# Optimization experiments

Measured on AMD Instinct MI355X. Metric: run time of the kernel, lower is better.

## Reference

```python
import jax, jax.numpy as jnp
import numpy as np

T, H, NH, NKV, HD = 2048, 1024, 16, 4, 64
I, E, TOPK = 2048, 8, 2
EPS = 1e-5
ROPE_BASE = 10000.0


def rms_norm(x, w):
    var = jnp.mean(x * x, axis=-1, keepdims=True)
    return x * jax.lax.rsqrt(var + EPS) * w


def apply_rope(x, positions, n_heads):
    # neox-style rotary over full head_dim
    t = x.reshape(-1, n_heads, HD)
    half = HD // 2
    inv_freq = 1.0 / (ROPE_BASE ** (jnp.arange(0, half, dtype=jnp.float32) / half))
    freqs = positions.astype(jnp.float32)[:, None] * inv_freq[None, :]  # [T, half]
    cos = jnp.cos(freqs)[:, None, :]
    sin = jnp.sin(freqs)[:, None, :]
    x1, x2 = t[..., :half], t[..., half:]
    rot = jnp.concatenate([x1 * cos - x2 * sin, x2 * cos + x1 * sin], axis=-1)
    return rot.reshape(x.shape)


def setup_inputs():
    key = jax.random.key(0)
    ks = jax.random.split(key, 9)
    s = 0.02
    return dict(
        positions=jnp.arange(T, dtype=jnp.int32),
        hidden_states=jax.random.normal(ks[0], (T, H), jnp.float32),
        input_ln_w=jnp.ones((H,), jnp.float32),
        post_ln_w=jnp.ones((H,), jnp.float32),
        residual_ln_w=jnp.ones((H,), jnp.float32),
        qkv_w=jax.random.normal(ks[1], ((NH + 2 * NKV) * HD, H), jnp.float32) * s,
        o_w=jax.random.normal(ks[2], (H, NH * HD), jnp.float32) * s,
        gate_w=jax.random.normal(ks[3], (E, H), jnp.float32) * s,
        ws=jax.random.normal(ks[4], (E, 2 * I, H), jnp.float32) * s,
        w2s=jax.random.normal(ks[5], (E, H, I), jnp.float32) * s,
        res_w13=jax.random.normal(ks[6], (2 * H, H), jnp.float32) * s,
        res_w2=jax.random.normal(ks[7], (H, H), jnp.float32) * s,
    )


def attention(x, positions, qkv_w, o_w):
    qkv = x @ qkv_w.T  # [T, (NH+2*NKV)*HD]
    q, k, v = jnp.split(qkv, [NH * HD, NH * HD + NKV * HD], axis=-1)
    q = apply_rope(q, positions, NH)
    k = apply_rope(k, positions, NKV)
    q = q.reshape(T, NH, HD)
    k = k.reshape(T, NKV, HD)
    v = v.reshape(T, NKV, HD)
    rep = NH // NKV  # GQA: repeat kv heads
    k = jnp.repeat(k, rep, axis=1)
    v = jnp.repeat(v, rep, axis=1)
    scale = HD ** -0.5
    scores = jnp.einsum('tnd,snd->nts', q, k) * scale  # [NH, T, T]
    causal = jnp.tril(jnp.ones((T, T), dtype=bool))
    scores = jnp.where(causal[None], scores, -jnp.inf)
    probs = jax.nn.softmax(scores, axis=-1)
    out = jnp.einsum('nts,snd->tnd', probs, v).reshape(T, NH * HD)
    return out @ o_w.T


def silu_and_mul(gu):
    g, u = jnp.split(gu, 2, axis=-1)
    return jax.nn.silu(g) * u


def moe(x, gate_w, ws, w2s):
    logits = x @ gate_w.T  # [T, E]
    probs = jax.nn.softmax(logits, axis=-1)
    topk_w, topk_ids = jax.lax.top_k(probs, TOPK)
    topk_w = topk_w / jnp.sum(topk_w, axis=-1, keepdims=True)  # renormalize (top_k > 1)
    routes = jnp.zeros((x.shape[0], E), x.dtype).at[
        jnp.arange(x.shape[0])[:, None], topk_ids].set(topk_w)  # [T, E] sparse routing
    gu = jnp.einsum('th,eih->tei', x, ws)        # [T, E, 2I]
    act = silu_and_mul(gu)                        # [T, E, I]
    eo = jnp.einsum('tei,ehi->teh', act, w2s)     # [T, E, H]
    return jnp.einsum('te,teh->th', routes, eo)


def reference(positions, hidden_states, input_ln_w, post_ln_w, residual_ln_w,
              qkv_w, o_w, gate_w, ws, w2s, res_w13, res_w2):
    residual_input = hidden_states
    h = rms_norm(hidden_states, input_ln_w)
    h = attention(h, positions, qkv_w, o_w)
    residual_attn = residual_input + h
    # parallel residual MLP branch (ffn_dim == hidden)
    r = rms_norm(residual_attn, residual_ln_w)
    r = silu_and_mul(r @ res_w13.T) @ res_w2.T
    residual_mlp = residual_attn + r
    # MoE branch
    m = rms_norm(residual_attn, post_ln_w)
    m = moe(m, gate_w, ws, w2s)
    return residual_mlp + m
```

## Files before the change

### kernel.cpp

```cpp
#include <hip/hip_runtime.h>
#include <stdint.h>


typedef _Float16 f16;
typedef _Float16 f16x8 __attribute__((ext_vector_type(8)));
typedef _Float16 f16x4 __attribute__((ext_vector_type(4)));
typedef float f32x4 __attribute__((ext_vector_type(4)));

#define DEV __device__ __forceinline__

DEV void glds16(const void* g, void* l) {
  __builtin_amdgcn_global_load_lds((const __attribute__((address_space(1))) void*)g,
                                   (__attribute__((address_space(3))) void*)l, 16, 0, 0);
}

__global__ void cvt_f16_kernel(const float* __restrict__ in, f16* __restrict__ outp) {
  const size_t i = ((size_t)blockIdx.x * 256 + threadIdx.x) * 4;
  float4 f = *(const float4*)(in + i);
  f16x4 o;
  o[0] = (f16)f.x; o[1] = (f16)f.y; o[2] = (f16)f.z; o[3] = (f16)f.w;
  *(f16x4*)(outp + i) = o;
}

__global__ void cvt_f16x2_kernel(const float* __restrict__ in,
                                 f16* __restrict__ oh, f16* __restrict__ ol) {
  const size_t i = ((size_t)blockIdx.x * 256 + threadIdx.x) * 4;
  float4 f = *(const float4*)(in + i);
  f16x4 h, l;
  h[0] = (f16)f.x; l[0] = (f16)(f.x - (float)h[0]);
  h[1] = (f16)f.y; l[1] = (f16)(f.y - (float)h[1]);
  h[2] = (f16)f.z; l[2] = (f16)(f.z - (float)h[2]);
  h[3] = (f16)f.w; l[3] = (f16)(f.w - (float)h[3]);
  *(f16x4*)(oh + i) = h;
  *(f16x4*)(ol + i) = l;
}

__global__ void rmsnorm_kernel(const float* __restrict__ in, const float* __restrict__ w,
                               f16* __restrict__ outp) {
  const int t = blockIdx.x * 4 + (threadIdx.x >> 6);
  const int lane = threadIdx.x & 63;
  const float* x = in + (size_t)t * 1024;
  float v[16]; float ss = 0.f;
#pragma unroll
  for (int j = 0; j < 16; j++) { float a = x[lane + 64 * j]; v[j] = a; ss += a * a; }
#pragma unroll
  for (int m = 1; m < 64; m <<= 1) ss += __shfl_xor(ss, m);
  const float rs = rsqrtf(ss * (1.f / 1024.f) + 1e-5f);
#pragma unroll
  for (int j = 0; j < 16; j++)
    outp[(size_t)t * 1024 + lane + 64 * j] = (f16)(v[j] * rs * w[lane + 64 * j]);
}

__global__ void rmsnorm_dual_kernel(const float* __restrict__ in,
                                    const float* __restrict__ w1, const float* __restrict__ w2,
                                    f16* __restrict__ o1, f16* __restrict__ o2) {
  const int t = blockIdx.x * 4 + (threadIdx.x >> 6);
  const int lane = threadIdx.x & 63;
  const float* x = in + (size_t)t * 1024;
  float v[16]; float ss = 0.f;
#pragma unroll
  for (int j = 0; j < 16; j++) { float a = x[lane + 64 * j]; v[j] = a; ss += a * a; }
#pragma unroll
  for (int m = 1; m < 64; m <<= 1) ss += __shfl_xor(ss, m);
  const float rs = rsqrtf(ss * (1.f / 1024.f) + 1e-5f);
#pragma unroll
  for (int j = 0; j < 16; j++) {
    float nv = v[j] * rs;
    size_t idx = (size_t)t * 1024 + lane + 64 * j;
    o1[idx] = (f16)(nv * w1[lane + 64 * j]);
    o2[idx] = (f16)(nv * w2[lane + 64 * j]);
  }
}

template <int EPI, int BN, int SPLITK = 1>
__global__ __launch_bounds__(256) void gemm_f16_kernel(
    const f16* __restrict__ A, const f16* __restrict__ B,
    void* __restrict__ outp, const float* __restrict__ addsrc,
    int M, int N, int K) {
  constexpr int JT = BN / 32;
  __shared__ __attribute__((aligned(16))) f16 As[2][128 * 32];
  __shared__ __attribute__((aligned(16))) f16 Bs[2][BN * 32];
  const int tid = threadIdx.x;
  const size_t row0 = (size_t)blockIdx.y * 128, col0 = (size_t)blockIdx.x * BN;
  const int ks = (SPLITK > 1) ? (int)blockIdx.z : 0;
  const int kspan = K / SPLITK, kb = ks * kspan;
  const int c0 = tid, c1 = tid + 256;
  const f16* a0 = A + (row0 + (c0 >> 2)) * K + (c0 & 3) * 8;
  const f16* a1 = A + (row0 + (c1 >> 2)) * K + (c1 & 3) * 8;
  const f16* b0 = B + (col0 + (c0 >> 2)) * K + (c0 & 3) * 8;
  const f16* b1 = B + (col0 + ((BN == 128) ? (c1 >> 2) : 0)) * K + (c1 & 3) * 8;

  const int wave = tid >> 6, lane = tid & 63, lr = lane >> 4, lc = lane & 15;
  const int wr = wave >> 1, wc = wave & 1;

  f32x4 acc[4][JT];
#pragma unroll
  for (int i = 0; i < 4; i++)
#pragma unroll
    for (int j = 0; j < JT; j++) acc[i][j] = (f32x4){0.f, 0.f, 0.f, 0.f};

  auto stage = [&](int k0, int buf) {
    glds16(a0 + k0, As[buf] + c0 * 8);
    glds16(a1 + k0, As[buf] + c1 * 8);
    glds16(b0 + k0, Bs[buf] + c0 * 8);
    if constexpr (BN == 128) glds16(b1 + k0, Bs[buf] + c1 * 8);
  };

  stage(kb, 0);
  __syncthreads();
  int cur = 0;
  for (int k0 = kb; k0 < kb + kspan; k0 += 32) {
    if (k0 + 32 < kb + kspan) stage(k0 + 32, cur ^ 1);
    f16x8 af[4], bfr[JT];
#pragma unroll
    for (int i = 0; i < 4; i++)
      af[i] = *(const f16x8*)(As[cur] + (wr * 64 + i * 16 + lc) * 32 + lr * 8);
#pragma unroll
    for (int j = 0; j < JT; j++)
      bfr[j] = *(const f16x8*)(Bs[cur] + (wc * (BN / 2) + j * 16 + lc) * 32 + lr * 8);
#pragma unroll
    for (int i = 0; i < 4; i++)
#pragma unroll
      for (int j = 0; j < JT; j++)
        acc[i][j] = __builtin_amdgcn_mfma_f32_16x16x32_f16(af[i], bfr[j], acc[i][j], 0, 0, 0);
    __syncthreads();
    cur ^= 1;
  }

#pragma unroll
  for (int i = 0; i < 4; i++)
#pragma unroll
    for (int j = 0; j < JT; j++) {
      const size_t rbase = row0 + wr * 64 + i * 16 + lr * 4;
      const size_t col = col0 + wc * (BN / 2) + j * 16 + lc;
#pragma unroll
      for (int r = 0; r < 4; r++) {
        size_t idx = (rbase + r) * N + col;
        if constexpr (SPLITK > 1) {
          ((float*)outp)[(size_t)ks * M * N + idx] = acc[i][j][r];
        } else if constexpr (EPI == 0) ((float*)outp)[idx] = acc[i][j][r];
        else if constexpr (EPI == 1) ((float*)outp)[idx] = acc[i][j][r] + addsrc[idx];
        else ((f16*)outp)[idx] = (f16)acc[i][j][r];
      }
    }
}

template <int SPLITK>
__global__ __launch_bounds__(256) void gemm_f16x2_add_kernel(
    const f16* __restrict__ Ah, const f16* __restrict__ Al,
    const f16* __restrict__ Bh, const f16* __restrict__ Bl,
    float* __restrict__ outp, const float* __restrict__ addsrc,
    int M, int N, int K) {
  __shared__ __attribute__((aligned(16))) f16 Ash[2][128 * 32];
  __shared__ __attribute__((aligned(16))) f16 Asl[2][128 * 32];
  __shared__ __attribute__((aligned(16))) f16 Bsh[2][64 * 32];
  __shared__ __attribute__((aligned(16))) f16 Bsl[2][64 * 32];
  const int tid = threadIdx.x;
  const size_t row0 = (size_t)blockIdx.y * 128, col0 = (size_t)blockIdx.x * 64;
  const int ks = (SPLITK > 1) ? (int)blockIdx.z : 0;
  const int kspan = K / SPLITK, kb = ks * kspan;
  const int c0 = tid, c1 = tid + 256;
  const size_t aoff0 = (row0 + (c0 >> 2)) * K + (c0 & 3) * 8;
  const size_t aoff1 = (row0 + (c1 >> 2)) * K + (c1 & 3) * 8;
  const size_t boff0 = (col0 + (c0 >> 2)) * K + (c0 & 3) * 8;

  const int wave = tid >> 6, lane = tid & 63, lr = lane >> 4, lc = lane & 15;
  const int wr = wave >> 1, wc = wave & 1;

  f32x4 acc[4][2];
#pragma unroll
  for (int i = 0; i < 4; i++)
#pragma unroll
    for (int j = 0; j < 2; j++) acc[i][j] = (f32x4){0.f, 0.f, 0.f, 0.f};

  auto stage = [&](int k0, int buf) {
    glds16(Ah + aoff0 + k0, Ash[buf] + c0 * 8);
    glds16(Ah + aoff1 + k0, Ash[buf] + c1 * 8);
    glds16(Al + aoff0 + k0, Asl[buf] + c0 * 8);
    glds16(Al + aoff1 + k0, Asl[buf] + c1 * 8);
    glds16(Bh + boff0 + k0, Bsh[buf] + c0 * 8);
    glds16(Bl + boff0 + k0, Bsl[buf] + c0 * 8);
  };

  stage(kb, 0);
  __syncthreads();
  int cur = 0;
  for (int k0 = kb; k0 < kb + kspan; k0 += 32) {
    if (k0 + 32 < kb + kspan) stage(k0 + 32, cur ^ 1);
    f16x8 afh[4], afl[4], bfh[2], bfl[2];
#pragma unroll
    for (int i = 0; i < 4; i++) {
      const int ro = (wr * 64 + i * 16 + lc) * 32 + lr * 8;
      afh[i] = *(const f16x8*)(Ash[cur] + ro);
      afl[i] = *(const f16x8*)(Asl[cur] + ro);
    }
#pragma unroll
    for (int j = 0; j < 2; j++) {
      const int ro = (wc * 32 + j * 16 + lc) * 32 + lr * 8;
      bfh[j] = *(const f16x8*)(Bsh[cur] + ro);
      bfl[j] = *(const f16x8*)(Bsl[cur] + ro);
    }
#pragma unroll
    for (int i = 0; i < 4; i++)
#pragma unroll
      for (int j = 0; j < 2; j++) {
        acc[i][j] = __builtin_amdgcn_mfma_f32_16x16x32_f16(afh[i], bfh[j], acc[i][j], 0, 0, 0);
        acc[i][j] = __builtin_amdgcn_mfma_f32_16x16x32_f16(afh[i], bfl[j], acc[i][j], 0, 0, 0);
        acc[i][j] = __builtin_amdgcn_mfma_f32_16x16x32_f16(afl[i], bfh[j], acc[i][j], 0, 0, 0);
      }
    __syncthreads();
    cur ^= 1;
  }

#pragma unroll
  for (int i = 0; i < 4; i++)
#pragma unroll
    for (int j = 0; j < 2; j++) {
      const size_t rbase = row0 + wr * 64 + i * 16 + lr * 4;
      const size_t col = col0 + wc * 32 + j * 16 + lc;
#pragma unroll
      for (int r = 0; r < 4; r++) {
        size_t idx = (rbase + r) * N + col;
        if constexpr (SPLITK > 1) outp[(size_t)ks * M * N + idx] = acc[i][j][r];
        else outp[idx] = acc[i][j][r] + addsrc[idx];
      }
    }
}

template <int DIVROW, int BN, int SPLITK = 1>
__global__ __launch_bounds__(256) void gemm_moe_kernel(
    const f16* __restrict__ A, const f16* __restrict__ Ball, void* __restrict__ outp,
    const int* __restrict__ perm, const int* __restrict__ counts,
    int N, int K, size_t strideB) {
  constexpr int JT = BN / 32;
  const int e = (int)blockIdx.z / SPLITK;
  const int ks = (int)blockIdx.z % SPLITK;
  const int cnt = counts[e];
  const int bm = blockIdx.y;
  if (bm * 128 >= cnt) return;
  const int kspan = K / SPLITK, kb = ks * kspan;
  const f16* B = Ball + (size_t)e * strideB;
  __shared__ __attribute__((aligned(16))) f16 As[2][128 * 32];
  __shared__ __attribute__((aligned(16))) f16 Bs[2][BN * 32];
  const int tid = threadIdx.x;
  const size_t col0 = (size_t)blockIdx.x * BN;
  const int c0 = tid, c1 = tid + 256;
  const int pbase = e * 2048 + bm * 128;
  const int rt0 = c0 >> 2, rt1 = c1 >> 2;
  const int sid0 = (bm * 128 + rt0 < cnt) ? perm[pbase + rt0] : -1;
  const int sid1 = (bm * 128 + rt1 < cnt) ? perm[pbase + rt1] : -1;
  const size_t ar0 = DIVROW ? (size_t)(sid0 >> 1) : (size_t)sid0;
  const size_t ar1 = DIVROW ? (size_t)(sid1 >> 1) : (size_t)sid1;
  const f16* ap0 = A + ar0 * K + (c0 & 3) * 8;
  const f16* ap1 = A + ar1 * K + (c1 & 3) * 8;
  const f16* b0 = B + (col0 + (c0 >> 2)) * K + (c0 & 3) * 8;
  const f16* b1 = B + (col0 + ((BN == 128) ? (c1 >> 2) : 0)) * K + (c1 & 3) * 8;

  const int wave = tid >> 6, lane = tid & 63, lr = lane >> 4, lc = lane & 15;
  const int wr = wave >> 1, wc = wave & 1;

  f32x4 acc[4][JT];
#pragma unroll
  for (int i = 0; i < 4; i++)
#pragma unroll
    for (int j = 0; j < JT; j++) acc[i][j] = (f32x4){0.f, 0.f, 0.f, 0.f};

  auto stageB = [&](int k0, int buf) {
    glds16(b0 + k0, Bs[buf] + c0 * 8);
    if constexpr (BN == 128) glds16(b1 + k0, Bs[buf] + c1 * 8);
  };
  auto loadA = [&](int k0, f16x8& va0, f16x8& va1) {
#pragma unroll
    for (int x = 0; x < 8; x++) { va0[x] = (f16)0.f; va1[x] = (f16)0.f; }
    if (sid0 >= 0) va0 = *(const f16x8*)(ap0 + k0);
    if (sid1 >= 0) va1 = *(const f16x8*)(ap1 + k0);
  };

  f16x8 va0, va1;
  loadA(kb, va0, va1);
  stageB(kb, 0);
  *(f16x8*)(As[0] + c0 * 8) = va0;
  *(f16x8*)(As[0] + c1 * 8) = va1;
  __syncthreads();
  int cur = 0;
  for (int k0 = kb; k0 < kb + kspan; k0 += 32) {
    const bool nxt = (k0 + 32 < kb + kspan);
    if (nxt) { stageB(k0 + 32, cur ^ 1); loadA(k0 + 32, va0, va1); }
    f16x8 af[4], bfr[JT];
#pragma unroll
    for (int i = 0; i < 4; i++)
      af[i] = *(const f16x8*)(As[cur] + (wr * 64 + i * 16 + lc) * 32 + lr * 8);
#pragma unroll
    for (int j = 0; j < JT; j++)
      bfr[j] = *(const f16x8*)(Bs[cur] + (wc * (BN / 2) + j * 16 + lc) * 32 + lr * 8);
#pragma unroll
    for (int i = 0; i < 4; i++)
#pragma unroll
      for (int j = 0; j < JT; j++)
        acc[i][j] = __builtin_amdgcn_mfma_f32_16x16x32_f16(af[i], bfr[j], acc[i][j], 0, 0, 0);
    if (nxt) {
      *(f16x8*)(As[cur ^ 1] + c0 * 8) = va0;
      *(f16x8*)(As[cur ^ 1] + c1 * 8) = va1;
    }
    __syncthreads();
    cur ^= 1;
  }

  int sids[4][4];
#pragma unroll
  for (int i = 0; i < 4; i++)
#pragma unroll
    for (int r = 0; r < 4; r++) {
      int rit = wr * 64 + i * 16 + lr * 4 + r;
      sids[i][r] = (bm * 128 + rit < cnt) ? perm[pbase + rit] : -1;
    }
#pragma unroll
  for (int i = 0; i < 4; i++)
#pragma unroll
    for (int j = 0; j < JT; j++) {
      const size_t col = col0 + wc * (BN / 2) + j * 16 + lc;
#pragma unroll
      for (int r = 0; r < 4; r++)
        if (sids[i][r] >= 0) {
          if constexpr (SPLITK > 1)
            ((float*)outp)[((size_t)ks * 4096 + sids[i][r]) * N + col] = acc[i][j][r];
          else
            ((f16*)outp)[(size_t)sids[i][r] * N + col] = (f16)acc[i][j][r];
        }
    }
}

__global__ void rope_kernel(const float* __restrict__ qkv, const int* __restrict__ pos,
                            f16* __restrict__ qr, f16* __restrict__ kr) {
  const int t = blockIdx.y;
  const int u = blockIdx.x * 256 + threadIdx.x;
  if (u >= 640) return;
  const float* b0 = qkv + (size_t)t * 1536;
  const float* b1 = b0 + (size_t)2048 * 1536;
  const int head = u >> 5, i = u & 31;
  const bool isq = head < 16;
  const int off = isq ? head * 64 + i : 1024 + (head - 16) * 64 + i;
  const float x1 = b0[off] + b1[off], x2 = b0[off + 32] + b1[off + 32];
  const double ph = (double)pos[t] * exp((double)i * -0.28782313662425575);
  const float c = (float)cos(ph), s = (float)sin(ph);
  const float r1 = x1 * c - x2 * s, r2 = x2 * c + x1 * s;
  if (isq) {
    const float qs = 0.18033688011116042f;
    qr[(size_t)t * 1024 + head * 64 + i] = (f16)(qs * r1);
    qr[(size_t)t * 1024 + head * 64 + i + 32] = (f16)(qs * r2);
  } else {
    const int kh = head - 16;
    kr[(size_t)t * 256 + kh * 64 + i] = (f16)r1;
    kr[(size_t)t * 256 + kh * 64 + i + 32] = (f16)r2;
  }
}

__global__ void vtrans_kernel(const float* __restrict__ qkvf, f16* __restrict__ vt) {
  __shared__ float Ts[64 * 69];
  const int t0 = blockIdx.x * 64;
  const int kv = blockIdx.y;
  const int tid = threadIdx.x;
  const int tr = tid >> 2, jj = tid & 3;
  const float* src0 = qkvf + (size_t)(t0 + tr) * 1536 + 1280 + kv * 64 + jj * 16;
  const float* src1 = src0 + (size_t)2048 * 1536;
#pragma unroll
  for (int x = 0; x < 4; x++) {
    float4 f = *(const float4*)(src0 + x * 4);
    float4 g = *(const float4*)(src1 + x * 4);
    Ts[tr * 69 + jj * 16 + x * 4 + 0] = f.x + g.x;
    Ts[tr * 69 + jj * 16 + x * 4 + 1] = f.y + g.y;
    Ts[tr * 69 + jj * 16 + x * 4 + 2] = f.z + g.z;
    Ts[tr * 69 + jj * 16 + x * 4 + 3] = f.w + g.w;
  }
  __syncthreads();
  f16* dst = vt + (size_t)(kv * 64 + tr) * 2048 + t0 + jj * 16;
#pragma unroll
  for (int x = 0; x < 2; x++) {
    f16x8 o;
#pragma unroll
    for (int i = 0; i < 8; i++) o[i] = (f16)Ts[(jj * 16 + x * 8 + i) * 69 + tr];
    *(f16x8*)(dst + x * 8) = o;
  }
}

__global__ void add3_kernel(float* __restrict__ o, const float* __restrict__ a,
                            const float* __restrict__ p0, const float* __restrict__ p1) {
  const size_t i4 = ((size_t)blockIdx.x * 256 + threadIdx.x) * 4;
  float4 va = *(const float4*)(a + i4);
  float4 v0 = *(const float4*)(p0 + i4);
  float4 v1 = *(const float4*)(p1 + i4);
  va.x += v0.x + v1.x;
  va.y += v0.y + v1.y;
  va.z += v0.z + v1.z;
  va.w += v0.w + v1.w;
  *(float4*)(o + i4) = va;
}

__global__ __launch_bounds__(256, 3) void attn_kernel(
    const f16* __restrict__ qr, const f16* __restrict__ kr, const f16* __restrict__ vt,
    f16* __restrict__ ahi, f16* __restrict__ alo) {
  const int qt = 31 - (int)blockIdx.x;
  const int h = blockIdx.y;
  const int kvh = h >> 2;
  __shared__ __attribute__((aligned(16))) f16 Ks[128 * 72];
  __shared__ __attribute__((aligned(16))) f16 Vs[64 * 136];
  __shared__ __attribute__((aligned(16))) f16 Pl[4 * 16 * 136];
  const int tid = threadIdx.x;
  const int wave = tid >> 6, lane = tid & 63, lr = lane >> 4, lc = lane & 15;
  const int trow = qt * 64 + wave * 16 + lc;
  f16* Pw = Pl + wave * 16 * 136;

  const int krow = tid >> 3, kcol = (tid & 7) * 8;
  const int vrow = tid >> 4, vcol = (tid & 15) * 8;
  const f16* kgbase = kr + (size_t)kvh * 64 + kcol;
  const f16* vgbase = vt + (size_t)(kvh * 64 + vrow) * 2048 + vcol;

  const f16* qp = qr + (size_t)trow * 1024 + h * 64 + lr * 8;
  f16x8 qf0 = *(const f16x8*)(qp);
  f16x8 qf1 = *(const f16x8*)(qp + 32);

  float m_run = -3e38f, l_run = 0.f;
  f32x4 accO[4];
#pragma unroll
  for (int jo = 0; jo < 4; jo++) accO[jo] = (f32x4){0.f, 0.f, 0.f, 0.f};

  const int nch = (qt >> 1) + 1;

  f16x8 kreg[4], vreg[4];
#pragma unroll
  for (int it = 0; it < 4; it++) {
    kreg[it] = *(const f16x8*)(kgbase + (size_t)(it * 32 + krow) * 256);
    vreg[it] = *(const f16x8*)(vgbase + it * 16 * 2048);
  }

  for (int ch = 0; ch < nch; ++ch) {
    const int c0 = ch * 128;
    const bool last = (ch == nch - 1);

    __syncthreads();
#pragma unroll
    for (int it = 0; it < 4; it++) {
      *(f16x8*)(Ks + (it * 32 + krow) * 72 + kcol) = kreg[it];
      *(f16x8*)(Vs + (it * 16 + vrow) * 136 + vcol) = vreg[it];
    }
    __syncthreads();

    if (!last) {
      const int c1 = c0 + 128;
#pragma unroll
      for (int it = 0; it < 4; it++) {
        kreg[it] = *(const f16x8*)(kgbase + (size_t)(c1 + it * 32 + krow) * 256);
        vreg[it] = *(const f16x8*)(vgbase + it * 16 * 2048 + c1);
      }
    }

    f32x4 st[8];
#pragma unroll
    for (int j = 0; j < 8; j++) {
      const f16* kp = Ks + (j * 16 + lc) * 72 + lr * 8;
      f16x8 ka0 = *(const f16x8*)(kp);
      f16x8 ka1 = *(const f16x8*)(kp + 32);
      f32x4 s = (f32x4){0.f, 0.f, 0.f, 0.f};
      s = __builtin_amdgcn_mfma_f32_16x16x32_f16(ka0, qf0, s, 0, 0, 0);
      s = __builtin_amdgcn_mfma_f32_16x16x32_f16(ka1, qf1, s, 0, 0, 0);
      st[j] = s;
    }

    if (last) {
#pragma unroll
      for (int j = 0; j < 8; j++)
#pragma unroll
        for (int r = 0; r < 4; r++)
          if (c0 + j * 16 + lr * 4 + r > trow) st[j][r] = -3e38f;
    }

    float mc = -3e38f;
#pragma unroll
    for (int j = 0; j < 8; j++)
      mc = fmaxf(mc, fmaxf(fmaxf(st[j][0], st[j][1]), fmaxf(st[j][2], st[j][3])));
    mc = fmaxf(mc, __shfl_xor(mc, 16));
    mc = fmaxf(mc, __shfl_xor(mc, 32));
    const float mn = fmaxf(m_run, mc);
    const float alpha = __builtin_amdgcn_exp2f(m_run - mn);
    m_run = mn;

    float ls = 0.f;
#pragma unroll
    for (int j = 0; j < 8; j++) {
      f16x4 pv;
#pragma unroll
      for (int r = 0; r < 4; r++) {
        float e = __builtin_amdgcn_exp2f(st[j][r] - mn);
        ls += e;
        pv[r] = (f16)e;
      }
      *(f16x4*)(Pw + lc * 136 + j * 16 + lr * 4) = pv;
    }
    ls += __shfl_xor(ls, 16);
    ls += __shfl_xor(ls, 32);
    l_run = l_run * alpha + ls;
#pragma unroll
    for (int jo = 0; jo < 4; jo++) accO[jo] *= alpha;

#pragma unroll
    for (int kkt = 0; kkt < 4; kkt++) {
      f16x8 pb = *(const f16x8*)(Pw + lc * 136 + kkt * 32 + lr * 8);
#pragma unroll
      for (int jo = 0; jo < 4; jo++) {
        f16x8 va = *(const f16x8*)(Vs + (jo * 16 + lc) * 136 + kkt * 32 + lr * 8);
        accO[jo] = __builtin_amdgcn_mfma_f32_16x16x32_f16(va, pb, accO[jo], 0, 0, 0);
      }
    }
  }

  const float inv = 1.f / l_run;
#pragma unroll
  for (int jo = 0; jo < 4; jo++) {
    f16x4 hi4, lo4;
#pragma unroll
    for (int r = 0; r < 4; r++) {
      float o = accO[jo][r] * inv;
      f16 hv = (f16)o;
      hi4[r] = hv;
      lo4[r] = (f16)(o - (float)hv);
    }
    const size_t idx = (size_t)trow * 1024 + h * 64 + jo * 16 + lr * 4;
    *(f16x4*)(ahi + idx) = hi4;
    *(f16x4*)(alo + idx) = lo4;
  }
}

__global__ void routing_kernel(const float* __restrict__ resA,
                               const float* __restrict__ postw,
                               const float* __restrict__ gw,
                               int* __restrict__ counts, int* __restrict__ perm,
                               float* __restrict__ rw) {
  const int t = blockIdx.x * 4 + (threadIdx.x >> 6);
  const int lane = threadIdx.x & 63;
  const float* x = resA + (size_t)t * 1024;
  float v[16]; float ss = 0.f;
#pragma unroll
  for (int j = 0; j < 16; j++) { float a = x[lane + 64 * j]; v[j] = a; ss += a * a; }
#pragma unroll
  for (int m = 1; m < 64; m <<= 1) ss += __shfl_xor(ss, m);
  const float rs = rsqrtf(ss * (1.f / 1024.f) + 1e-5f);
#pragma unroll
  for (int j = 0; j < 16; j++) v[j] *= rs * postw[lane + 64 * j];
  float lg[8];
#pragma unroll
  for (int e = 0; e < 8; e++) {
    float p = 0.f;
    const float* g = gw + (size_t)e * 1024;
#pragma unroll
    for (int j = 0; j < 16; j++) p += v[j] * g[lane + 64 * j];
#pragma unroll
    for (int m = 1; m < 64; m <<= 1) p += __shfl_xor(p, m);
    lg[e] = p;
  }
  if (lane == 0) {
    int e0 = 0; float b0 = lg[0];
#pragma unroll
    for (int e = 1; e < 8; e++) if (lg[e] > b0) { b0 = lg[e]; e0 = e; }
    int e1 = -1; float b1 = -3e38f;
#pragma unroll
    for (int e = 0; e < 8; e++) if (e != e0 && lg[e] > b1) { b1 = lg[e]; e1 = e; }
    const float w0 = 1.f / (1.f + expf(b1 - b0));
    const float w1 = 1.f - w0;
    int p0 = atomicAdd(&counts[e0], 1);
    perm[e0 * 2048 + p0] = t * 2;
    int p1 = atomicAdd(&counts[e1], 1);
    perm[e1 * 2048 + p1] = t * 2 + 1;
    rw[t * 2] = w0;
    rw[t * 2 + 1] = w1;
  }
}

__global__ void silu_mul_kernel(const f16* __restrict__ gu, f16* __restrict__ outp, int lgN) {
  const int N = 1 << lgN;
  const size_t i4 = ((size_t)blockIdx.x * 256 + threadIdx.x) * 4;
  const size_t r = i4 >> lgN;
  const int c = (int)(i4 & (N - 1));
  const f16* gp = gu + r * (size_t)(2 * N) + c;
  f16x4 g = *(const f16x4*)gp;
  f16x4 u = *(const f16x4*)(gp + N);
  f16x4 o;
#pragma unroll
  for (int x = 0; x < 4; x++) {
    float gg = (float)g[x], uu = (float)u[x];
    o[x] = (f16)(gg / (1.f + __expf(-gg)) * uu);
  }
  *(f16x4*)(outp + r * (size_t)N + c) = o;
}

__global__ void final_add4_kernel(float* __restrict__ outp, const float* __restrict__ eo4,
                                  const float* __restrict__ rw) {
  const size_t i4 = ((size_t)blockIdx.x * 256 + threadIdx.x) * 4;
  const int t = (int)(i4 >> 10);
  const int c = (int)(i4 & 1023);
  const float w0 = rw[2 * t], w1 = rw[2 * t + 1];
  float4 s0 = {0.f, 0.f, 0.f, 0.f}, s1 = {0.f, 0.f, 0.f, 0.f};
#pragma unroll
  for (int ks = 0; ks < 4; ks++) {
    const float* p = eo4 + (size_t)ks * 4096 * 1024;
    float4 a = *(const float4*)(p + (size_t)(2 * t) * 1024 + c);
    float4 b = *(const float4*)(p + (size_t)(2 * t + 1) * 1024 + c);
    s0.x += a.x; s0.y += a.y; s0.z += a.z; s0.w += a.w;
    s1.x += b.x; s1.y += b.y; s1.z += b.z; s1.w += b.w;
  }
  float4 o = *(float4*)(outp + i4);
  o.x += w0 * s0.x + w1 * s1.x;
  o.y += w0 * s0.y + w1 * s1.y;
  o.z += w0 * s0.z + w1 * s1.z;
  o.w += w0 * s0.w + w1 * s1.w;
  *(float4*)(outp + i4) = o;
}

extern "C" void kernel_launch(void* const* d_in, const int* in_sizes, int n_in,
                              void* d_out, int out_size, void* d_ws, size_t ws_size,
                              hipStream_t stream) {
  const int* positions = (const int*)d_in[0];
  const float* hidden = (const float*)d_in[1];
  const float* in_ln = (const float*)d_in[2];
  const float* post_ln = (const float*)d_in[3];
  const float* res_ln = (const float*)d_in[4];
  const float* qkv_w = (const float*)d_in[5];
  const float* o_w = (const float*)d_in[6];
  const float* gate_w = (const float*)d_in[7];
  const float* ws_w = (const float*)d_in[8];
  const float* w2s_w = (const float*)d_in[9];
  const float* w13_w = (const float*)d_in[10];
  const float* w2_w = (const float*)d_in[11];
  float* out = (float*)d_out;

  char* p = (char*)d_ws;
  auto alloc = [&](size_t b) { void* r = (void*)p; p += (b + 255) & ~(size_t)255; return r; };

  f16* wqkv = (f16*)alloc((size_t)1536 * 1024 * 2);
  f16* woh  = (f16*)alloc((size_t)1024 * 1024 * 2);
  f16* wol  = (f16*)alloc((size_t)1024 * 1024 * 2);
  f16* wws  = (f16*)alloc((size_t)8 * 4096 * 1024 * 2);
  f16* ww2  = (f16*)alloc((size_t)8 * 1024 * 2048 * 2);
  f16* w13  = (f16*)alloc((size_t)2048 * 1024 * 2);
  f16* w2c  = (f16*)alloc((size_t)1024 * 1024 * 2);
  f16* hn   = (f16*)alloc((size_t)2048 * 1024 * 2);
  float* qkvp = (float*)alloc((size_t)2 * 2048 * 1536 * 4);
  f16* qr = (f16*)alloc((size_t)2048 * 1024 * 2);
  f16* kr = (f16*)alloc((size_t)2048 * 256 * 2);
  f16* vt = (f16*)alloc((size_t)256 * 2048 * 2);
  f16* ath = (f16*)alloc((size_t)2048 * 1024 * 2);
  f16* atl = (f16*)alloc((size_t)2048 * 1024 * 2);
  float* opp = (float*)alloc((size_t)2 * 2048 * 1024 * 4);
  float* resA = (float*)alloc((size_t)2048 * 1024 * 4);
  f16* rn = (f16*)alloc((size_t)2048 * 1024 * 2);
  f16* mn = (f16*)alloc((size_t)2048 * 1024 * 2);
  f16* gu13 = (f16*)alloc((size_t)2048 * 2048 * 2);
  f16* act13 = (f16*)alloc((size_t)2048 * 1024 * 2);
  float* w2p = (float*)alloc((size_t)2 * 2048 * 1024 * 4);
  f16* gum = (f16*)alloc((size_t)4096 * 4096 * 2);
  f16* actm = (f16*)alloc((size_t)4096 * 2048 * 2);
  float* eo4 = (float*)alloc((size_t)4 * 4096 * 1024 * 4);
  float* rw = (float*)alloc((size_t)4096 * 4);
  int* counts = (int*)alloc(256);
  int* perm = (int*)alloc((size_t)8 * 2048 * 4);

  cvt_f16_kernel<<<dim3(1536 * 1024 / 1024), dim3(256), 0, stream>>>(qkv_w, wqkv);
  cvt_f16_kernel<<<dim3(8 * 4096 * 1024 / 1024), dim3(256), 0, stream>>>(ws_w, wws);
  cvt_f16_kernel<<<dim3(8 * 1024 * 2048 / 1024), dim3(256), 0, stream>>>(w2s_w, ww2);
  cvt_f16_kernel<<<dim3(2048 * 1024 / 1024), dim3(256), 0, stream>>>(w13_w, w13);
  cvt_f16_kernel<<<dim3(1024 * 1024 / 1024), dim3(256), 0, stream>>>(w2_w, w2c);
  cvt_f16x2_kernel<<<dim3(1024 * 1024 / 1024), dim3(256), 0, stream>>>(o_w, woh, wol);
  hipMemsetAsync(counts, 0, 256, stream);

  rmsnorm_kernel<<<dim3(512), dim3(256), 0, stream>>>(hidden, in_ln, hn);
  gemm_f16_kernel<0, 64, 2><<<dim3(24, 16, 2), dim3(256), 0, stream>>>(
      hn, wqkv, (void*)qkvp, (const float*)nullptr, 2048, 1536, 1024);
  rope_kernel<<<dim3(3, 2048), dim3(256), 0, stream>>>(qkvp, positions, qr, kr);
  vtrans_kernel<<<dim3(32, 4), dim3(256), 0, stream>>>(qkvp, vt);
  attn_kernel<<<dim3(32, 16), dim3(256), 0, stream>>>(qr, kr, vt, ath, atl);
  gemm_f16x2_add_kernel<2><<<dim3(16, 16, 2), dim3(256), 0, stream>>>(
      ath, atl, woh, wol, opp, (const float*)nullptr, 2048, 1024, 1024);
  add3_kernel<<<dim3(2048), dim3(256), 0, stream>>>(
      resA, hidden, opp, opp + (size_t)2048 * 1024);

  rmsnorm_dual_kernel<<<dim3(512), dim3(256), 0, stream>>>(resA, res_ln, post_ln, rn, mn);
  routing_kernel<<<dim3(512), dim3(256), 0, stream>>>(resA, post_ln, gate_w, counts, perm, rw);

  gemm_f16_kernel<2, 64><<<dim3(32, 16), dim3(256), 0, stream>>>(
      rn, w13, (void*)gu13, (const float*)nullptr, 2048, 2048, 1024);
  silu_mul_kernel<<<dim3(2048 * 1024 / 1024), dim3(256), 0, stream>>>(gu13, act13, 10);
  gemm_f16_kernel<0, 64, 2><<<dim3(16, 16, 2), dim3(256), 0, stream>>>(
      act13, w2c, (void*)w2p, (const float*)nullptr, 2048, 1024, 1024);
  add3_kernel<<<dim3(2048), dim3(256), 0, stream>>>(
      out, resA, w2p, w2p + (size_t)2048 * 1024);

  gemm_moe_kernel<1, 128><<<dim3(32, 16, 8), dim3(256), 0, stream>>>(
      mn, wws, (void*)gum, perm, counts, 4096, 1024, (size_t)4096 * 1024);
  silu_mul_kernel<<<dim3(4096 * 2048 / 1024), dim3(256), 0, stream>>>(gum, actm, 11);
  gemm_moe_kernel<0, 128, 4><<<dim3(8, 16, 32), dim3(256), 0, stream>>>(
      actm, ww2, (void*)eo4, perm, counts, 1024, 2048, (size_t)1024 * 2048);
  final_add4_kernel<<<dim3(2048 * 1024 / 1024), dim3(256), 0, stream>>>(out, eo4, rw);
}
```

Before: 642.8 us.

## Deepen GEMM pipelines to multi-stage LDS buffering with XOR swizzle

```diff
diff --git a/kernel.cpp b/kernel.cpp
--- a/kernel.cpp
+++ b/kernel.cpp
@@ -78,20 +78,25 @@
     void* __restrict__ outp, const float* __restrict__ addsrc,
     int M, int N, int K) {
   constexpr int JT = BN / 32;
-  __shared__ __attribute__((aligned(16))) f16 As[2][128 * 32];
-  __shared__ __attribute__((aligned(16))) f16 Bs[2][BN * 32];
+  constexpr int L = (BN == 128) ? 4 : 3;
+  __shared__ __attribute__((aligned(16))) f16 As[4][128 * 32];
+  __shared__ __attribute__((aligned(16))) f16 Bs[4][BN * 32];
   const int tid = threadIdx.x;
   const size_t row0 = (size_t)blockIdx.y * 128, col0 = (size_t)blockIdx.x * BN;
   const int ks = (SPLITK > 1) ? (int)blockIdx.z : 0;
   const int kspan = K / SPLITK, kb = ks * kspan;
+  const int nt = kspan >> 5;
   const int c0 = tid, c1 = tid + 256;
-  const f16* a0 = A + (row0 + (c0 >> 2)) * K + (c0 & 3) * 8;
-  const f16* a1 = A + (row0 + (c1 >> 2)) * K + (c1 & 3) * 8;
-  const f16* b0 = B + (col0 + (c0 >> 2)) * K + (c0 & 3) * 8;
-  const f16* b1 = B + (col0 + ((BN == 128) ? (c1 >> 2) : 0)) * K + (c1 & 3) * 8;
+  const int sw0 = ((c0 & 3) ^ ((c0 >> 3) & 3)) * 8;
+  const int sw1 = ((c1 & 3) ^ ((c1 >> 3) & 3)) * 8;
+  const f16* a0 = A + (row0 + (c0 >> 2)) * K + sw0;
+  const f16* a1 = A + (row0 + (c1 >> 2)) * K + sw1;
+  const f16* b0 = B + (col0 + (c0 >> 2)) * K + sw0;
+  const f16* b1 = B + (col0 + ((BN == 128) ? (c1 >> 2) : 0)) * K + ((BN == 128) ? sw1 : 0);
 
   const int wave = tid >> 6, lane = tid & 63, lr = lane >> 4, lc = lane & 15;
   const int wr = wave >> 1, wc = wave & 1;
+  const int rsw = (lr ^ ((lc >> 1) & 3)) * 8;
 
   f32x4 acc[4][JT];
 #pragma unroll
@@ -106,25 +111,28 @@
     if constexpr (BN == 128) glds16(b1 + k0, Bs[buf] + c1 * 8);
   };
 
-  stage(kb, 0);
-  __syncthreads();
-  int cur = 0;
-  for (int k0 = kb; k0 < kb + kspan; k0 += 32) {
-    if (k0 + 32 < kb + kspan) stage(k0 + 32, cur ^ 1);
+  stage(kb, 0); stage(kb + 32, 1); stage(kb + 64, 2);
+  for (int t = 0; t < nt; ++t) {
+    if (t <= nt - 3)      asm volatile("s_waitcnt vmcnt(%0)" :: "n"(2 * L) : "memory");
+    else if (t == nt - 2) asm volatile("s_waitcnt vmcnt(%0)" :: "n"(L) : "memory");
+    else                  asm volatile("s_waitcnt vmcnt(0)" ::: "memory");
+    __builtin_amdgcn_s_barrier();
+    asm volatile("" ::: "memory");
+    if (t + 3 < nt) stage(kb + (t + 3) * 32, (t + 3) & 3);
+    const f16* Ab = As[t & 3];
+    const f16* Bb = Bs[t & 3];
     f16x8 af[4], bfr[JT];
 #pragma unroll
     for (int i = 0; i < 4; i++)
-      af[i] = *(const f16x8*)(As[cur] + (wr * 64 + i * 16 + lc) * 32 + lr * 8);
+      af[i] = *(const f16x8*)(Ab + (wr * 64 + i * 16 + lc) * 32 + rsw);
 #pragma unroll
     for (int j = 0; j < JT; j++)
-      bfr[j] = *(const f16x8*)(Bs[cur] + (wc * (BN / 2) + j * 16 + lc) * 32 + lr * 8);
+      bfr[j] = *(const f16x8*)(Bb + (wc * (BN / 2) + j * 16 + lc) * 32 + rsw);
 #pragma unroll
     for (int i = 0; i < 4; i++)
 #pragma unroll
       for (int j = 0; j < JT; j++)
         acc[i][j] = __builtin_amdgcn_mfma_f32_16x16x32_f16(af[i], bfr[j], acc[i][j], 0, 0, 0);
-    __syncthreads();
-    cur ^= 1;
   }
 
 #pragma unroll
@@ -151,21 +159,25 @@
     const f16* __restrict__ Bh, const f16* __restrict__ Bl,
     float* __restrict__ outp, const float* __restrict__ addsrc,
     int M, int N, int K) {
-  __shared__ __attribute__((aligned(16))) f16 Ash[2][128 * 32];
-  __shared__ __attribute__((aligned(16))) f16 Asl[2][128 * 32];
-  __shared__ __attribute__((aligned(16))) f16 Bsh[2][64 * 32];
-  __shared__ __attribute__((aligned(16))) f16 Bsl[2][64 * 32];
+  __shared__ __attribute__((aligned(16))) f16 Ash[3][128 * 32];
+  __shared__ __attribute__((aligned(16))) f16 Asl[3][128 * 32];
+  __shared__ __attribute__((aligned(16))) f16 Bsh[3][64 * 32];
+  __shared__ __attribute__((aligned(16))) f16 Bsl[3][64 * 32];
   const int tid = threadIdx.x;
   const size_t row0 = (size_t)blockIdx.y * 128, col0 = (size_t)blockIdx.x * 64;
   const int ks = (SPLITK > 1) ? (int)blockIdx.z : 0;
   const int kspan = K / SPLITK, kb = ks * kspan;
+  const int nt = kspan >> 5;
   const int c0 = tid, c1 = tid + 256;
-  const size_t aoff0 = (row0 + (c0 >> 2)) * K + (c0 & 3) * 8;
-  const size_t aoff1 = (row0 + (c1 >> 2)) * K + (c1 & 3) * 8;
-  const size_t boff0 = (col0 + (c0 >> 2)) * K + (c0 & 3) * 8;
+  const int sw0 = ((c0 & 3) ^ ((c0 >> 3) & 3)) * 8;
+  const int sw1 = ((c1 & 3) ^ ((c1 >> 3) & 3)) * 8;
+  const size_t aoff0 = (row0 + (c0 >> 2)) * K + sw0;
+  const size_t aoff1 = (row0 + (c1 >> 2)) * K + sw1;
+  const size_t boff0 = (col0 + (c0 >> 2)) * K + sw0;
 
   const int wave = tid >> 6, lane = tid & 63, lr = lane >> 4, lc = lane & 15;
   const int wr = wave >> 1, wc = wave & 1;
+  const int rsw = (lr ^ ((lc >> 1) & 3)) * 8;
 
   f32x4 acc[4][2];
 #pragma unroll
@@ -182,23 +194,26 @@
     glds16(Bl + boff0 + k0, Bsl[buf] + c0 * 8);
   };
 
-  stage(kb, 0);
-  __syncthreads();
-  int cur = 0;
-  for (int k0 = kb; k0 < kb + kspan; k0 += 32) {
-    if (k0 + 32 < kb + kspan) stage(k0 + 32, cur ^ 1);
+  stage(kb, 0); stage(kb + 32, 1);
+  int bc = 0, bs = 2;
+  for (int t = 0; t < nt; ++t) {
+    if (t <= nt - 2) asm volatile("s_waitcnt vmcnt(%0)" :: "n"(6) : "memory");
+    else             asm volatile("s_waitcnt vmcnt(0)" ::: "memory");
+    __builtin_amdgcn_s_barrier();
+    asm volatile("" ::: "memory");
+    if (t + 2 < nt) stage(kb + (t + 2) * 32, bs);
     f16x8 afh[4], afl[4], bfh[2], bfl[2];
 #pragma unroll
     for (int i = 0; i < 4; i++) {
-      const int ro = (wr * 64 + i * 16 + lc) * 32 + lr * 8;
-      afh[i] = *(const f16x8*)(Ash[cur] + ro);
-      afl[i] = *(const f16x8*)(Asl[cur] + ro);
+      const int ro = (wr * 64 + i * 16 + lc) * 32 + rsw;
+      afh[i] = *(const f16x8*)(Ash[bc] + ro);
+      afl[i] = *(const f16x8*)(Asl[bc] + ro);
     }
 #pragma unroll
     for (int j = 0; j < 2; j++) {
-      const int ro = (wc * 32 + j * 16 + lc) * 32 + lr * 8;
-      bfh[j] = *(const f16x8*)(Bsh[cur] + ro);
-      bfl[j] = *(const f16x8*)(Bsl[cur] + ro);
+      const int ro = (wc * 32 + j * 16 + lc) * 32 + rsw;
+      bfh[j] = *(const f16x8*)(Bsh[bc] + ro);
+      bfl[j] = *(const f16x8*)(Bsl[bc] + ro);
     }
 #pragma unroll
     for (int i = 0; i < 4; i++)
@@ -208,8 +223,8 @@
         acc[i][j] = __builtin_amdgcn_mfma_f32_16x16x32_f16(afh[i], bfl[j], acc[i][j], 0, 0, 0);
         acc[i][j] = __builtin_amdgcn_mfma_f32_16x16x32_f16(afl[i], bfh[j], acc[i][j], 0, 0, 0);
       }
-    __syncthreads();
-    cur ^= 1;
+    bc = (bc == 2) ? 0 : bc + 1;
+    bs = (bs == 2) ? 0 : bs + 1;
   }
 
 #pragma unroll
@@ -233,31 +248,36 @@
     const int* __restrict__ perm, const int* __restrict__ counts,
     int N, int K, size_t strideB) {
   constexpr int JT = BN / 32;
+  constexpr int L = (BN == 128) ? 4 : 3;
   const int e = (int)blockIdx.z / SPLITK;
   const int ks = (int)blockIdx.z % SPLITK;
   const int cnt = counts[e];
   const int bm = blockIdx.y;
   if (bm * 128 >= cnt) return;
   const int kspan = K / SPLITK, kb = ks * kspan;
+  const int nt = kspan >> 5;
   const f16* B = Ball + (size_t)e * strideB;
-  __shared__ __attribute__((aligned(16))) f16 As[2][128 * 32];
-  __shared__ __attribute__((aligned(16))) f16 Bs[2][BN * 32];
+  __shared__ __attribute__((aligned(16))) f16 As[4][128 * 32];
+  __shared__ __attribute__((aligned(16))) f16 Bs[4][BN * 32];
   const int tid = threadIdx.x;
   const size_t col0 = (size_t)blockIdx.x * BN;
   const int c0 = tid, c1 = tid + 256;
   const int pbase = e * 2048 + bm * 128;
   const int rt0 = c0 >> 2, rt1 = c1 >> 2;
-  const int sid0 = (bm * 128 + rt0 < cnt) ? perm[pbase + rt0] : -1;
-  const int sid1 = (bm * 128 + rt1 < cnt) ? perm[pbase + rt1] : -1;
+  const int sid0 = (bm * 128 + rt0 < cnt) ? perm[pbase + rt0] : 0;
+  const int sid1 = (bm * 128 + rt1 < cnt) ? perm[pbase + rt1] : 0;
   const size_t ar0 = DIVROW ? (size_t)(sid0 >> 1) : (size_t)sid0;
   const size_t ar1 = DIVROW ? (size_t)(sid1 >> 1) : (size_t)sid1;
-  const f16* ap0 = A + ar0 * K + (c0 & 3) * 8;
-  const f16* ap1 = A + ar1 * K + (c1 & 3) * 8;
-  const f16* b0 = B + (col0 + (c0 >> 2)) * K + (c0 & 3) * 8;
-  const f16* b1 = B + (col0 + ((BN == 128) ? (c1 >> 2) : 0)) * K + (c1 & 3) * 8;
+  const int sw0 = ((c0 & 3) ^ ((c0 >> 3) & 3)) * 8;
+  const int sw1 = ((c1 & 3) ^ ((c1 >> 3) & 3)) * 8;
+  const f16* ap0 = A + ar0 * K + sw0;
+  const f16* ap1 = A + ar1 * K + sw1;
+  const f16* b0 = B + (col0 + (c0 >> 2)) * K + sw0;
+  const f16* b1 = B + (col0 + ((BN == 128) ? (c1 >> 2) : 0)) * K + ((BN == 128) ? sw1 : 0);
 
   const int wave = tid >> 6, lane = tid & 63, lr = lane >> 4, lc = lane & 15;
   const int wr = wave >> 1, wc = wave & 1;
+  const int rsw = (lr ^ ((lc >> 1) & 3)) * 8;
 
   f32x4 acc[4][JT];
 #pragma unroll
@@ -265,45 +285,35 @@
 #pragma unroll
     for (int j = 0; j < JT; j++) acc[i][j] = (f32x4){0.f, 0.f, 0.f, 0.f};
 
-  auto stageB = [&](int k0, int buf) {
+  auto stage = [&](int k0, int buf) {
+    glds16(ap0 + k0, As[buf] + c0 * 8);
+    glds16(ap1 + k0, As[buf] + c1 * 8);
     glds16(b0 + k0, Bs[buf] + c0 * 8);
     if constexpr (BN == 128) glds16(b1 + k0, Bs[buf] + c1 * 8);
   };
-  auto loadA = [&](int k0, f16x8& va0, f16x8& va1) {
-#pragma unroll
-    for (int x = 0; x < 8; x++) { va0[x] = (f16)0.f; va1[x] = (f16)0.f; }
-    if (sid0 >= 0) va0 = *(const f16x8*)(ap0 + k0);
-    if (sid1 >= 0) va1 = *(const f16x8*)(ap1 + k0);
-  };
-
-  f16x8 va0, va1;
-  loadA(kb, va0, va1);
-  stageB(kb, 0);
-  *(f16x8*)(As[0] + c0 * 8) = va0;
-  *(f16x8*)(As[0] + c1 * 8) = va1;
-  __syncthreads();
-  int cur = 0;
-  for (int k0 = kb; k0 < kb + kspan; k0 += 32) {
-    const bool nxt = (k0 + 32 < kb + kspan);
-    if (nxt) { stageB(k0 + 32, cur ^ 1); loadA(k0 + 32, va0, va1); }
+
+  stage(kb, 0); stage(kb + 32, 1); stage(kb + 64, 2);
+  for (int t = 0; t < nt; ++t) {
+    if (t <= nt - 3)      asm volatile("s_waitcnt vmcnt(%0)" :: "n"(2 * L) : "memory");
+    else if (t == nt - 2) asm volatile("s_waitcnt vmcnt(%0)" :: "n"(L) : "memory");
+    else                  asm volatile("s_waitcnt vmcnt(0)" ::: "memory");
+    __builtin_amdgcn_s_barrier();
+    asm volatile("" ::: "memory");
+    if (t + 3 < nt) stage(kb + (t + 3) * 32, (t + 3) & 3);
+    const f16* Ab = As[t & 3];
+    const f16* Bb = Bs[t & 3];
     f16x8 af[4], bfr[JT];
 #pragma unroll
     for (int i = 0; i < 4; i++)
-      af[i] = *(const f16x8*)(As[cur] + (wr * 64 + i * 16 + lc) * 32 + lr * 8);
+      af[i] = *(const f16x8*)(Ab + (wr * 64 + i * 16 + lc) * 32 + rsw);
 #pragma unroll
     for (int j = 0; j < JT; j++)
-      bfr[j] = *(const f16x8*)(Bs[cur] + (wc * (BN / 2) + j * 16 + lc) * 32 + lr * 8);
+      bfr[j] = *(const f16x8*)(Bb + (wc * (BN / 2) + j * 16 + lc) * 32 + rsw);
 #pragma unroll
     for (int i = 0; i < 4; i++)
 #pragma unroll
       for (int j = 0; j < JT; j++)
         acc[i][j] = __builtin_amdgcn_mfma_f32_16x16x32_f16(af[i], bfr[j], acc[i][j], 0, 0, 0);
-    if (nxt) {
-      *(f16x8*)(As[cur ^ 1] + c0 * 8) = va0;
-      *(f16x8*)(As[cur ^ 1] + c1 * 8) = va1;
-    }
-    __syncthreads();
-    cur ^= 1;
   }
 
   int sids[4][4];
```

Measured after the change: 650.3 us. About the same (+1.2%).
